# Kernel tuning notes

Measured on AMD Instinct MI355X. Metric: run time of the kernel, lower is better.

The kernel has to match this reference:

```python
import jax, jax.numpy as jnp
import numpy as np

N_NODES = 40000
N_EDGES = 640000
IN_DIM = 256
HID = 128
EMB = 128


def _mean_agg(h, src, dst, n):
    # PyG SimpleConv(aggr='mean'): out[i] = mean_{(j->i) in E} h[j]; 0 if no in-edges
    s = jax.ops.segment_sum(h[src], dst, num_segments=n)              # [N, D]
    deg = jax.ops.segment_sum(jnp.ones((src.shape[0],), h.dtype), dst,
                              num_segments=n)                          # [N]
    return s / jnp.maximum(deg, 1.0)[:, None]


def setup_inputs() -> dict:
    key = jax.random.key(0)
    ks = jax.random.split(key, 10)
    scale_in = 1.0 / np.sqrt(IN_DIM)
    scale_mix = 1.0 / np.sqrt(2 * HID)
    scale_out = 1.0 / np.sqrt(HID)
    return {
        "x": jax.random.normal(ks[0], (N_NODES, IN_DIM), dtype=jnp.float32),
        "W_in": jax.random.uniform(ks[1], (IN_DIM, HID), jnp.float32, -scale_in, scale_in),
        "b_in": jnp.zeros((HID,), jnp.float32),
        "W_mix0": jax.random.uniform(ks[2], (2 * HID, HID), jnp.float32, -scale_mix, scale_mix),
        "b_mix0": jnp.zeros((HID,), jnp.float32),
        "W_mix1": jax.random.uniform(ks[3], (2 * HID, HID), jnp.float32, -scale_mix, scale_mix),
        "b_mix1": jnp.zeros((HID,), jnp.float32),
        "W_out": jax.random.uniform(ks[4], (HID, EMB), jnp.float32, -scale_out, scale_out),
        "b_out": jnp.zeros((EMB,), jnp.float32),
        "edge_index": jax.random.randint(ks[5], (2, N_EDGES), 0, N_NODES, dtype=jnp.int64 if jax.config.jax_enable_x64 else jnp.int32),
    }


def reference(x, W_in, b_in, W_mix0, b_mix0, W_mix1, b_mix1, W_out, b_out, edge_index):
    src, dst = edge_index[0], edge_index[1]
    n = x.shape[0]
    # eval mode: dropout is identity
    h = jax.nn.relu(x @ W_in + b_in)                                   # [N, HID]
    for i, (W_mix, b_mix) in enumerate([(W_mix0, b_mix0), (W_mix1, b_mix1)]):
        h1 = _mean_agg(h, src, dst, n)                                 # 1-hop mean
        h2 = _mean_agg(h1, src, dst, n)                                # 2-hop mean
        h = jnp.concatenate([h1, h2], axis=-1) @ W_mix + b_mix         # [N, HID]
        if i != 1:
            h = jax.nn.relu(h)
    return h @ W_out + b_out                                           # [N, EMB]
```

## Files before the change

kernel.cpp:

```cpp
#include <hip/hip_runtime.h>

#define N_NODES 40000
#define N_EDGES 640000
#define IN_DIM 256
#define HID 128

typedef short bf16x8 __attribute__((ext_vector_type(8)));
typedef float f32x4 __attribute__((ext_vector_type(4)));

__device__ __forceinline__ unsigned short f2bf(float f) {
    unsigned int u = __float_as_uint(f);
    unsigned int r = (u + 0x7FFFu + ((u >> 16) & 1u)) >> 16;
    return (unsigned short)r;
}
__device__ __forceinline__ float bf2f(unsigned short b) {
    return __uint_as_float(((unsigned int)b) << 16);
}


__global__ __launch_bounds__(256) void front_kernel(
    const int* __restrict__ dst, int* __restrict__ deg, int E,
    const float* __restrict__ W0, const float* __restrict__ W1,
    const float* __restrict__ W2, const float* __restrict__ W3,
    unsigned short* __restrict__ H0, unsigned short* __restrict__ L0,
    unsigned short* __restrict__ H1, unsigned short* __restrict__ L1,
    unsigned short* __restrict__ H2, unsigned short* __restrict__ L2,
    unsigned short* __restrict__ H3, unsigned short* __restrict__ L3) {
    int bid = blockIdx.x;
    if (bid < 2500) {
        int e = bid * 256 + threadIdx.x;
        if (e < E) atomicAdd(&deg[dst[e]], 1);
        return;
    }
    int i = (bid - 2500) * 256 + threadIdx.x;
    const float* W;
    unsigned short *H, *L;
    int local;
    if (i < 32768)       { W = W0; H = H0; L = L0; local = i; }
    else if (i < 65536)  { W = W1; H = H1; L = L1; local = i - 32768; }
    else if (i < 98304)  { W = W2; H = H2; L = L2; local = i - 65536; }
    else if (i < 114688) { W = W3; H = H3; L = L3; local = i - 98304; }
    else return;
    int k = local >> 7, c = local & 127;
    float w = W[local];
    unsigned short h = f2bf(w);
    unsigned short l = f2bf(w - bf2f(h));
    int d = (k >> 5) * 4096 + c * 32 + (k & 31);
    H[d] = h;
    L[d] = l;
}


__global__ __launch_bounds__(1024) void write_offsets(const int* __restrict__ deg,
                                                      int* __restrict__ row_off,
                                                      int* __restrict__ cursor, int N) {
    __shared__ int sh[1024];
    int tid = threadIdx.x;
    int bid = blockIdx.x;
    int limit = bid << 10;
    int psum = 0;
    for (int j = tid * 4; j < limit; j += 4096) {
        int4 v = *(const int4*)&deg[j];
        psum += v.x + v.y + v.z + v.w;
    }
    sh[tid] = psum;
    __syncthreads();
#pragma unroll
    for (int o = 512; o > 0; o >>= 1) {
        if (tid < o) sh[tid] += sh[tid + o];
        __syncthreads();
    }
    int base = sh[0];
    __syncthreads();
    int i = limit + tid;
    int v = (i < N) ? deg[i] : 0;
    sh[tid] = v;
    __syncthreads();
#pragma unroll
    for (int off = 1; off < 1024; off <<= 1) {
        int t = (tid >= off) ? sh[tid - off] : 0;
        __syncthreads();
        sh[tid] += t;
        __syncthreads();
    }
    int excl = sh[tid] - v + base;
    if (i < N) {
        row_off[i] = excl;
        cursor[i] = excl;
    }
    if (i == N - 1) row_off[N] = excl + v;
}


__global__ __launch_bounds__(256) void scatter_gemm1(
    const int* __restrict__ src, const int* __restrict__ dst,
    int* __restrict__ cursor, int* __restrict__ csr, int E,
    const float* __restrict__ x,
    const unsigned short* __restrict__ Bth, const unsigned short* __restrict__ Btl,
    const float* __restrict__ bias, unsigned short* __restrict__ Cbf) {
    int bid = blockIdx.x;
    if (bid >= 625) {
        int e = (bid - 625) * 256 + threadIdx.x;
        if (e < E) {
            int p = atomicAdd(&cursor[dst[e]], 1);
            csr[p] = src[e];
        }
        return;
    }
    __shared__ unsigned short Ah[64 * 32], Al[64 * 32];
    __shared__ unsigned short Bh[128 * 32], Bl[128 * 32];
    int tid = threadIdx.x;
    int lane = tid & 63, wid = tid >> 6;
    int wr = wid >> 1, wc = wid & 1;
    int row0 = bid * 64;

    f32x4 acc[2][4];
#pragma unroll
    for (int rt = 0; rt < 2; ++rt)
#pragma unroll
        for (int ct = 0; ct < 4; ++ct) acc[rt][ct] = 0.f;

    for (int s = 0; s < 8; ++s) {
        int kbase = s * 32;
#pragma unroll
        for (int i = 0; i < 2; ++i) {
            int cch = tid + i * 256;
            int r = cch >> 3, q = cch & 7;
            float4 v = *(const float4*)&x[(size_t)(row0 + r) * IN_DIM + kbase + q * 4];
            ushort4 hh, ll;
            hh.x = f2bf(v.x); ll.x = f2bf(v.x - bf2f(hh.x));
            hh.y = f2bf(v.y); ll.y = f2bf(v.y - bf2f(hh.y));
            hh.z = f2bf(v.z); ll.z = f2bf(v.z - bf2f(hh.z));
            hh.w = f2bf(v.w); ll.w = f2bf(v.w - bf2f(hh.w));
            *(ushort4*)&Ah[r * 32 + q * 4] = hh;
            *(ushort4*)&Al[r * 32 + q * 4] = ll;
        }
        {
            const float4* sh4 = (const float4*)(Bth + s * 4096);
            const float4* sl4 = (const float4*)(Btl + s * 4096);
            float4* dh4 = (float4*)Bh;
            float4* dl4 = (float4*)Bl;
            dh4[tid] = sh4[tid];
            dh4[tid + 256] = sh4[tid + 256];
            dl4[tid] = sl4[tid];
            dl4[tid + 256] = sl4[tid + 256];
        }
        __syncthreads();

        bf16x8 afh[2], afl[2], bfh[4], bfl[4];
#pragma unroll
        for (int rt = 0; rt < 2; ++rt) {
            int off = (wr * 32 + rt * 16 + (lane & 15)) * 32 + (lane >> 4) * 8;
            afh[rt] = *(const bf16x8*)&Ah[off];
            afl[rt] = *(const bf16x8*)&Al[off];
        }
#pragma unroll
        for (int ct = 0; ct < 4; ++ct) {
            int off = (wc * 64 + ct * 16 + (lane & 15)) * 32 + (lane >> 4) * 8;
            bfh[ct] = *(const bf16x8*)&Bh[off];
            bfl[ct] = *(const bf16x8*)&Bl[off];
        }
#pragma unroll
        for (int rt = 0; rt < 2; ++rt)
#pragma unroll
            for (int ct = 0; ct < 4; ++ct) {
                acc[rt][ct] = __builtin_amdgcn_mfma_f32_16x16x32_bf16(afh[rt], bfh[ct], acc[rt][ct], 0, 0, 0);
                acc[rt][ct] = __builtin_amdgcn_mfma_f32_16x16x32_bf16(afh[rt], bfl[ct], acc[rt][ct], 0, 0, 0);
                acc[rt][ct] = __builtin_amdgcn_mfma_f32_16x16x32_bf16(afl[rt], bfh[ct], acc[rt][ct], 0, 0, 0);
            }
        __syncthreads();
    }

#pragma unroll
    for (int ct = 0; ct < 4; ++ct) {
        int col = wc * 64 + ct * 16 + (lane & 15);
        float bv = bias[col];
#pragma unroll
        for (int rt = 0; rt < 2; ++rt) {
#pragma unroll
            for (int r = 0; r < 4; ++r) {
                int row = row0 + wr * 32 + rt * 16 + (lane >> 4) * 4 + r;
                float v = fmaxf(acc[rt][ct][r] + bv, 0.f);
                Cbf[(size_t)row * 128 + col] = f2bf(v);
            }
        }
    }
}


__global__ __launch_bounds__(256) void agg_mean_bf(const unsigned short* __restrict__ hbf,
                                                   const int* __restrict__ row_off,
                                                   const int* __restrict__ csr,
                                                   unsigned short* __restrict__ out_bf,
                                                   int N) {
    int node = blockIdx.x * 4 + (threadIdx.x >> 6);
    if (node >= N) return;
    int lane = threadIdx.x & 63;
    int half = lane >> 5;
    int sub = lane & 31;
    int beg = row_off[node], end = row_off[node + 1];
    float4 a0 = make_float4(0.f, 0.f, 0.f, 0.f);
    float4 a1 = make_float4(0.f, 0.f, 0.f, 0.f);
    int e = beg;
    for (; e + 7 < end; e += 8) {
        int s0 = csr[e + half];
        int s1 = csr[e + 2 + half];
        int s2 = csr[e + 4 + half];
        int s3 = csr[e + 6 + half];
        ushort4 u0 = *(const ushort4*)&hbf[(size_t)s0 * HID + sub * 4];
        ushort4 u1 = *(const ushort4*)&hbf[(size_t)s1 * HID + sub * 4];
        ushort4 u2 = *(const ushort4*)&hbf[(size_t)s2 * HID + sub * 4];
        ushort4 u3 = *(const ushort4*)&hbf[(size_t)s3 * HID + sub * 4];
        a0.x += bf2f(u0.x) + bf2f(u2.x);
        a0.y += bf2f(u0.y) + bf2f(u2.y);
        a0.z += bf2f(u0.z) + bf2f(u2.z);
        a0.w += bf2f(u0.w) + bf2f(u2.w);
        a1.x += bf2f(u1.x) + bf2f(u3.x);
        a1.y += bf2f(u1.y) + bf2f(u3.y);
        a1.z += bf2f(u1.z) + bf2f(u3.z);
        a1.w += bf2f(u1.w) + bf2f(u3.w);
    }
    for (; e + half < end; e += 2) {
        int s = csr[e + half];
        ushort4 u = *(const ushort4*)&hbf[(size_t)s * HID + sub * 4];
        a0.x += bf2f(u.x);
        a0.y += bf2f(u.y);
        a0.z += bf2f(u.z);
        a0.w += bf2f(u.w);
    }
    float4 acc;
    acc.x = a0.x + a1.x;
    acc.y = a0.y + a1.y;
    acc.z = a0.z + a1.z;
    acc.w = a0.w + a1.w;
    acc.x += __shfl_xor(acc.x, 32);
    acc.y += __shfl_xor(acc.y, 32);
    acc.z += __shfl_xor(acc.z, 32);
    acc.w += __shfl_xor(acc.w, 32);
    if (half == 0) {
        float inv = 1.0f / fmaxf((float)(end - beg), 1.0f);
        ushort4 ub;
        ub.x = f2bf(acc.x * inv);
        ub.y = f2bf(acc.y * inv);
        ub.z = f2bf(acc.z * inv);
        ub.w = f2bf(acc.w * inv);
        *(ushort4*)&out_bf[(size_t)node * HID + sub * 4] = ub;
    }
}


template <bool RELU>
__global__ __launch_bounds__(256) void gemm_a16(
    const unsigned short* __restrict__ A0, const unsigned short* __restrict__ A1,
    const unsigned short* __restrict__ Bth, const unsigned short* __restrict__ Btl,
    const float* __restrict__ bias, unsigned short* __restrict__ Cbf) {
    __shared__ unsigned short Ab[64 * 32];
    __shared__ unsigned short Bh[128 * 32], Bl[128 * 32];
    int tid = threadIdx.x;
    int lane = tid & 63, wid = tid >> 6;
    int wr = wid >> 1, wc = wid & 1;
    int row0 = blockIdx.x * 64;

    f32x4 acc[2][4];
#pragma unroll
    for (int rt = 0; rt < 2; ++rt)
#pragma unroll
        for (int ct = 0; ct < 4; ++ct) acc[rt][ct] = 0.f;

    for (int s = 0; s < 8; ++s) {
        const unsigned short* Asrc = (s < 4) ? A0 : A1;
        int kbase = (s & 3) * 32;
        {
            int r = tid >> 2, q = (tid & 3) * 8;
            *(float4*)&Ab[r * 32 + q] =
                *(const float4*)&Asrc[(size_t)(row0 + r) * HID + kbase + q];
        }
        {
            const float4* sh4 = (const float4*)(Bth + s * 4096);
            const float4* sl4 = (const float4*)(Btl + s * 4096);
            float4* dh4 = (float4*)Bh;
            float4* dl4 = (float4*)Bl;
            dh4[tid] = sh4[tid];
            dh4[tid + 256] = sh4[tid + 256];
            dl4[tid] = sl4[tid];
            dl4[tid + 256] = sl4[tid + 256];
        }
        __syncthreads();

        bf16x8 af[2], bfh[4], bfl[4];
#pragma unroll
        for (int rt = 0; rt < 2; ++rt) {
            int off = (wr * 32 + rt * 16 + (lane & 15)) * 32 + (lane >> 4) * 8;
            af[rt] = *(const bf16x8*)&Ab[off];
        }
#pragma unroll
        for (int ct = 0; ct < 4; ++ct) {
            int off = (wc * 64 + ct * 16 + (lane & 15)) * 32 + (lane >> 4) * 8;
            bfh[ct] = *(const bf16x8*)&Bh[off];
            bfl[ct] = *(const bf16x8*)&Bl[off];
        }
#pragma unroll
        for (int rt = 0; rt < 2; ++rt)
#pragma unroll
            for (int ct = 0; ct < 4; ++ct) {
                acc[rt][ct] = __builtin_amdgcn_mfma_f32_16x16x32_bf16(af[rt], bfh[ct], acc[rt][ct], 0, 0, 0);
                acc[rt][ct] = __builtin_amdgcn_mfma_f32_16x16x32_bf16(af[rt], bfl[ct], acc[rt][ct], 0, 0, 0);
            }
        __syncthreads();
    }

#pragma unroll
    for (int ct = 0; ct < 4; ++ct) {
        int col = wc * 64 + ct * 16 + (lane & 15);
        float bv = bias[col];
#pragma unroll
        for (int rt = 0; rt < 2; ++rt) {
#pragma unroll
            for (int r = 0; r < 4; ++r) {
                int row = row0 + wr * 32 + rt * 16 + (lane >> 4) * 4 + r;
                float v = acc[rt][ct][r] + bv;
                if (RELU) v = fmaxf(v, 0.f);
                Cbf[(size_t)row * 128 + col] = f2bf(v);
            }
        }
    }
}


__global__ __launch_bounds__(256) void gemm_mix_out(
    const unsigned short* __restrict__ A0, const unsigned short* __restrict__ A1,
    const unsigned short* __restrict__ BmH, const unsigned short* __restrict__ BmL,
    const float* __restrict__ bias_m,
    const unsigned short* __restrict__ BoH, const unsigned short* __restrict__ BoL,
    const float* __restrict__ bias_o, float* __restrict__ out) {
    __shared__ unsigned short Ab[64 * 32];
    __shared__ unsigned short Bh[128 * 32], Bl[128 * 32];
    __shared__ unsigned short AoH[4][64 * 32], AoL[4][64 * 32];
    int tid = threadIdx.x;
    int lane = tid & 63, wid = tid >> 6;
    int wr = wid >> 1, wc = wid & 1;
    int row0 = blockIdx.x * 64;

    f32x4 acc[2][4];
#pragma unroll
    for (int rt = 0; rt < 2; ++rt)
#pragma unroll
        for (int ct = 0; ct < 4; ++ct) acc[rt][ct] = 0.f;

    for (int s = 0; s < 8; ++s) {
        const unsigned short* Asrc = (s < 4) ? A0 : A1;
        int kbase = (s & 3) * 32;
        {
            int r = tid >> 2, q = (tid & 3) * 8;
            *(float4*)&Ab[r * 32 + q] =
                *(const float4*)&Asrc[(size_t)(row0 + r) * HID + kbase + q];
        }
        {
            const float4* sh4 = (const float4*)(BmH + s * 4096);
            const float4* sl4 = (const float4*)(BmL + s * 4096);
            float4* dh4 = (float4*)Bh;
            float4* dl4 = (float4*)Bl;
            dh4[tid] = sh4[tid];
            dh4[tid + 256] = sh4[tid + 256];
            dl4[tid] = sl4[tid];
            dl4[tid + 256] = sl4[tid + 256];
        }
        __syncthreads();

        bf16x8 af[2], bfh[4], bfl[4];
#pragma unroll
        for (int rt = 0; rt < 2; ++rt) {
            int off = (wr * 32 + rt * 16 + (lane & 15)) * 32 + (lane >> 4) * 8;
            af[rt] = *(const bf16x8*)&Ab[off];
        }
#pragma unroll
        for (int ct = 0; ct < 4; ++ct) {
            int off = (wc * 64 + ct * 16 + (lane & 15)) * 32 + (lane >> 4) * 8;
            bfh[ct] = *(const bf16x8*)&Bh[off];
            bfl[ct] = *(const bf16x8*)&Bl[off];
        }
#pragma unroll
        for (int rt = 0; rt < 2; ++rt)
#pragma unroll
            for (int ct = 0; ct < 4; ++ct) {
                acc[rt][ct] = __builtin_amdgcn_mfma_f32_16x16x32_bf16(af[rt], bfh[ct], acc[rt][ct], 0, 0, 0);
                acc[rt][ct] = __builtin_amdgcn_mfma_f32_16x16x32_bf16(af[rt], bfl[ct], acc[rt][ct], 0, 0, 0);
            }
        __syncthreads();
    }

#pragma unroll
    for (int ct = 0; ct < 4; ++ct) {
        int c = wc * 64 + ct * 16 + (lane & 15);
        int sp = c >> 5, cc = c & 31;
        float bv = bias_m[c];
#pragma unroll
        for (int rt = 0; rt < 2; ++rt) {
#pragma unroll
            for (int r = 0; r < 4; ++r) {
                int rl = wr * 32 + rt * 16 + (lane >> 4) * 4 + r;
                float v = acc[rt][ct][r] + bv;
                unsigned short h = f2bf(v);
                unsigned short l = f2bf(v - bf2f(h));
                AoH[sp][rl * 32 + cc] = h;
                AoL[sp][rl * 32 + cc] = l;
            }
        }
    }

#pragma unroll
    for (int rt = 0; rt < 2; ++rt)
#pragma unroll
        for (int ct = 0; ct < 4; ++ct) acc[rt][ct] = 0.f;

    for (int s = 0; s < 4; ++s) {
        {
            const float4* sh4 = (const float4*)(BoH + s * 4096);
            const float4* sl4 = (const float4*)(BoL + s * 4096);
            float4* dh4 = (float4*)Bh;
            float4* dl4 = (float4*)Bl;
            dh4[tid] = sh4[tid];
            dh4[tid + 256] = sh4[tid + 256];
            dl4[tid] = sl4[tid];
            dl4[tid + 256] = sl4[tid + 256];
        }
        __syncthreads();

        bf16x8 afh[2], afl[2], bfh[4], bfl[4];
#pragma unroll
        for (int rt = 0; rt < 2; ++rt) {
            int off = (wr * 32 + rt * 16 + (lane & 15)) * 32 + (lane >> 4) * 8;
            afh[rt] = *(const bf16x8*)&AoH[s][off];
            afl[rt] = *(const bf16x8*)&AoL[s][off];
        }
#pragma unroll
        for (int ct = 0; ct < 4; ++ct) {
            int off = (wc * 64 + ct * 16 + (lane & 15)) * 32 + (lane >> 4) * 8;
            bfh[ct] = *(const bf16x8*)&Bh[off];
            bfl[ct] = *(const bf16x8*)&Bl[off];
        }
#pragma unroll
        for (int rt = 0; rt < 2; ++rt)
#pragma unroll
            for (int ct = 0; ct < 4; ++ct) {
                acc[rt][ct] = __builtin_amdgcn_mfma_f32_16x16x32_bf16(afh[rt], bfh[ct], acc[rt][ct], 0, 0, 0);
                acc[rt][ct] = __builtin_amdgcn_mfma_f32_16x16x32_bf16(afh[rt], bfl[ct], acc[rt][ct], 0, 0, 0);
                acc[rt][ct] = __builtin_amdgcn_mfma_f32_16x16x32_bf16(afl[rt], bfh[ct], acc[rt][ct], 0, 0, 0);
            }
        __syncthreads();
    }

#pragma unroll
    for (int ct = 0; ct < 4; ++ct) {
        int col = wc * 64 + ct * 16 + (lane & 15);
        float bv = bias_o[col];
#pragma unroll
        for (int rt = 0; rt < 2; ++rt) {
#pragma unroll
            for (int r = 0; r < 4; ++r) {
                int row = row0 + wr * 32 + rt * 16 + (lane >> 4) * 4 + r;
                out[(size_t)row * 128 + col] = acc[rt][ct][r] + bv;
            }
        }
    }
}


extern "C" void kernel_launch(void* const* d_in, const int* in_sizes, int n_in,
                              void* d_out, int out_size, void* d_ws, size_t ws_size,
                              hipStream_t stream) {
    const float* x     = (const float*)d_in[0];
    const float* W_in  = (const float*)d_in[1];
    const float* b_in  = (const float*)d_in[2];
    const float* W_m0  = (const float*)d_in[3];
    const float* b_m0  = (const float*)d_in[4];
    const float* W_m1  = (const float*)d_in[5];
    const float* b_m1  = (const float*)d_in[6];
    const float* W_o   = (const float*)d_in[7];
    const float* b_o   = (const float*)d_in[8];
    const int*   eidx  = (const int*)d_in[9];
    const int* src = eidx;
    const int* dst = eidx + N_EDGES;

    char* ws = (char*)d_ws;
    size_t off = 0;
    auto alloc = [&](size_t bytes) -> char* {
        char* p = ws + off;
        off += (bytes + 255) & ~(size_t)255;
        return p;
    };
    int* deg     = (int*)alloc((size_t)N_NODES * 4);
    int* row_off = (int*)alloc((size_t)(N_NODES + 1) * 4);
    int* cursor  = (int*)alloc((size_t)N_NODES * 4);
    int* csr     = (int*)alloc((size_t)N_EDGES * 4);
    unsigned short* hbf1 = (unsigned short*)alloc((size_t)N_NODES * HID * 2);
    unsigned short* hbf2 = (unsigned short*)alloc((size_t)N_NODES * HID * 2);
    unsigned short* hbf3 = (unsigned short*)alloc((size_t)N_NODES * HID * 2);
    unsigned short* WinH = (unsigned short*)alloc(32768 * 2);
    unsigned short* WinL = (unsigned short*)alloc(32768 * 2);
    unsigned short* Wm0H = (unsigned short*)alloc(32768 * 2);
    unsigned short* Wm0L = (unsigned short*)alloc(32768 * 2);
    unsigned short* Wm1H = (unsigned short*)alloc(32768 * 2);
    unsigned short* Wm1L = (unsigned short*)alloc(32768 * 2);
    unsigned short* WoH  = (unsigned short*)alloc(16384 * 2);
    unsigned short* WoL  = (unsigned short*)alloc(16384 * 2);
    (void)ws_size;

    const int NB = (N_NODES + 1023) / 1024;

    hipMemsetAsync(deg, 0, (size_t)N_NODES * 4, stream);
    front_kernel<<<2500 + 448, 256, 0, stream>>>(dst, deg, N_EDGES,
                                                 W_in, W_m0, W_m1, W_o,
                                                 WinH, WinL, Wm0H, Wm0L,
                                                 Wm1H, Wm1L, WoH, WoL);
    write_offsets<<<NB, 1024, 0, stream>>>(deg, row_off, cursor, N_NODES);

    scatter_gemm1<<<625 + 2500, 256, 0, stream>>>(src, dst, cursor, csr, N_EDGES,
                                                  x, WinH, WinL, b_in, hbf1);

    agg_mean_bf<<<10000, 256, 0, stream>>>(hbf1, row_off, csr, hbf2, N_NODES);
    agg_mean_bf<<<10000, 256, 0, stream>>>(hbf2, row_off, csr, hbf3, N_NODES);
    gemm_a16<true><<<625, 256, 0, stream>>>(hbf2, hbf3, Wm0H, Wm0L, b_m0, hbf1);

    agg_mean_bf<<<10000, 256, 0, stream>>>(hbf1, row_off, csr, hbf2, N_NODES);
    agg_mean_bf<<<10000, 256, 0, stream>>>(hbf2, row_off, csr, hbf3, N_NODES);

    gemm_mix_out<<<625, 256, 0, stream>>>(hbf2, hbf3, Wm1H, Wm1L, b_m1,
                                          WoH, WoL, b_o, (float*)d_out);
}
```

Measured before the change: 217.3 us.

## Build CSR via two-level bucketed counting sort instead of per-node global atomics

Replaces the per-edge global atomic degree count, the full-node scan and the per-edge global atomic scatter with a two-level bucket sort. Edges are first counted into 313 buckets of 128 destination nodes using shared-memory atomics, then scattered into a packed staging array. A per-bucket finalize kernel sorts each bucket locally to build row offsets and the CSR. This cuts contended global atomics and random global writes, at the cost of an extra kernel, a staging buffer, and packing src into 16 bits, which relies on N_NODES fitting in 16 bits.

```diff
diff --git a/kernel.cpp b/kernel.cpp
--- a/kernel.cpp
+++ b/kernel.cpp
@@ -4,6 +4,7 @@
 #define N_EDGES 640000
 #define IN_DIM 256
 #define HID 128
+#define NBUCK 313
 
 typedef short bf16x8 __attribute__((ext_vector_type(8)));
 typedef float f32x4 __attribute__((ext_vector_type(4)));
@@ -18,21 +19,28 @@
 }
 
 
-__global__ __launch_bounds__(256) void front_kernel(
-    const int* __restrict__ dst, int* __restrict__ deg, int E,
+__global__ __launch_bounds__(256) void count_prep(
+    const int* __restrict__ dst, int* __restrict__ gbcnt, int E,
     const float* __restrict__ W0, const float* __restrict__ W1,
     const float* __restrict__ W2, const float* __restrict__ W3,
     unsigned short* __restrict__ H0, unsigned short* __restrict__ L0,
     unsigned short* __restrict__ H1, unsigned short* __restrict__ L1,
     unsigned short* __restrict__ H2, unsigned short* __restrict__ L2,
     unsigned short* __restrict__ H3, unsigned short* __restrict__ L3) {
-    int bid = blockIdx.x;
-    if (bid < 2500) {
-        int e = bid * 256 + threadIdx.x;
-        if (e < E) atomicAdd(&deg[dst[e]], 1);
+    int bid = blockIdx.x, tid = threadIdx.x;
+    if (bid < 157) {
+        __shared__ int cnt[NBUCK];
+        for (int j = tid; j < NBUCK; j += 256) cnt[j] = 0;
+        __syncthreads();
+        int base = bid * 4096;
+        int lim = min(base + 4096, E);
+        for (int i = base + tid; i < lim; i += 256) atomicAdd(&cnt[dst[i] >> 7], 1);
+        __syncthreads();
+        for (int j = tid; j < NBUCK; j += 256)
+            if (cnt[j]) atomicAdd(&gbcnt[j], cnt[j]);
         return;
     }
-    int i = (bid - 2500) * 256 + threadIdx.x;
+    int i = (bid - 157) * 256 + tid;
     const float* W;
     unsigned short *H, *L;
     int local;
@@ -51,65 +59,63 @@
 }
 
 
-__global__ __launch_bounds__(1024) void write_offsets(const int* __restrict__ deg,
-                                                      int* __restrict__ row_off,
-                                                      int* __restrict__ cursor, int N) {
-    __shared__ int sh[1024];
+__global__ __launch_bounds__(512) void scan_buckets(const int* __restrict__ gbcnt,
+                                                    int* __restrict__ bbase,
+                                                    int* __restrict__ bcursor,
+                                                    int* __restrict__ row_off) {
+    __shared__ int sh[512];
     int tid = threadIdx.x;
-    int bid = blockIdx.x;
-    int limit = bid << 10;
-    int psum = 0;
-    for (int j = tid * 4; j < limit; j += 4096) {
-        int4 v = *(const int4*)&deg[j];
-        psum += v.x + v.y + v.z + v.w;
-    }
-    sh[tid] = psum;
-    __syncthreads();
-#pragma unroll
-    for (int o = 512; o > 0; o >>= 1) {
-        if (tid < o) sh[tid] += sh[tid + o];
-        __syncthreads();
-    }
-    int base = sh[0];
-    __syncthreads();
-    int i = limit + tid;
-    int v = (i < N) ? deg[i] : 0;
+    int v = (tid < NBUCK) ? gbcnt[tid] : 0;
     sh[tid] = v;
     __syncthreads();
 #pragma unroll
-    for (int off = 1; off < 1024; off <<= 1) {
+    for (int off = 1; off < 512; off <<= 1) {
         int t = (tid >= off) ? sh[tid - off] : 0;
         __syncthreads();
         sh[tid] += t;
         __syncthreads();
     }
-    int excl = sh[tid] - v + base;
-    if (i < N) {
-        row_off[i] = excl;
-        cursor[i] = excl;
-    }
-    if (i == N - 1) row_off[N] = excl + v;
+    int excl = sh[tid] - v;
+    if (tid < NBUCK) {
+        bbase[tid] = excl;
+        bcursor[tid] = excl;
+    }
+    if (tid == NBUCK - 1) bbase[NBUCK] = excl + v;
+    if (tid == 0) row_off[N_NODES] = N_EDGES;
 }
 
 
 __global__ __launch_bounds__(256) void scatter_gemm1(
     const int* __restrict__ src, const int* __restrict__ dst,
-    int* __restrict__ cursor, int* __restrict__ csr, int E,
+    int* __restrict__ bcursor, unsigned int* __restrict__ stage, int E,
     const float* __restrict__ x,
     const unsigned short* __restrict__ Bth, const unsigned short* __restrict__ Btl,
     const float* __restrict__ bias, unsigned short* __restrict__ Cbf) {
     int bid = blockIdx.x;
+    int tid = threadIdx.x;
     if (bid >= 625) {
-        int e = (bid - 625) * 256 + threadIdx.x;
-        if (e < E) {
-            int p = atomicAdd(&cursor[dst[e]], 1);
-            csr[p] = src[e];
+        __shared__ int cnt[NBUCK];
+        int b2 = bid - 625;
+        for (int j = tid; j < NBUCK; j += 256) cnt[j] = 0;
+        __syncthreads();
+        int base = b2 * 4096;
+        int lim = min(base + 4096, E);
+        for (int i = base + tid; i < lim; i += 256) atomicAdd(&cnt[dst[i] >> 7], 1);
+        __syncthreads();
+        for (int j = tid; j < NBUCK; j += 256) {
+            int c = cnt[j];
+            if (c) cnt[j] = atomicAdd(&bcursor[j], c);
+        }
+        __syncthreads();
+        for (int i = base + tid; i < lim; i += 256) {
+            unsigned int d = (unsigned int)dst[i];
+            int p = atomicAdd(&cnt[d >> 7], 1);
+            stage[p] = (d << 16) | (unsigned int)src[i];
         }
         return;
     }
     __shared__ unsigned short Ah[64 * 32], Al[64 * 32];
     __shared__ unsigned short Bh[128 * 32], Bl[128 * 32];
-    int tid = threadIdx.x;
     int lane = tid & 63, wid = tid >> 6;
     int wr = wid >> 1, wc = wid & 1;
     int row0 = bid * 64;
@@ -184,6 +190,45 @@
                 Cbf[(size_t)row * 128 + col] = f2bf(v);
             }
         }
+    }
+}
+
+
+__global__ __launch_bounds__(256) void finalize_csr(const unsigned int* __restrict__ stage,
+                                                    const int* __restrict__ bbase,
+                                                    int* __restrict__ row_off,
+                                                    int* __restrict__ csr) {
+    __shared__ int ncnt[128];
+    __shared__ int s2[128];
+    int b = blockIdx.x, tid = threadIdx.x;
+    int nbase = b << 7;
+    int ncount = min(128, N_NODES - nbase);
+    int ebase = bbase[b], eend = bbase[b + 1];
+    if (tid < 128) ncnt[tid] = 0;
+    __syncthreads();
+    for (int i = ebase + tid; i < eend; i += 256)
+        atomicAdd(&ncnt[(stage[i] >> 16) & 127], 1);
+    __syncthreads();
+    if (tid < 128) s2[tid] = ncnt[tid];
+    __syncthreads();
+#pragma unroll
+    for (int off = 1; off < 128; off <<= 1) {
+        int t = (tid < 128 && tid >= off) ? s2[tid - off] : 0;
+        __syncthreads();
+        if (tid < 128) s2[tid] += t;
+        __syncthreads();
+    }
+    if (tid < 128) {
+        int excl = s2[tid] - ncnt[tid];
+        if (tid < ncount) row_off[nbase + tid] = ebase + excl;
+        ncnt[tid] = excl;
+    }
+    __syncthreads();
+    for (int i = ebase + tid; i < eend; i += 256) {
+        unsigned int ent = stage[i];
+        int loc = (ent >> 16) & 127;
+        int p = atomicAdd(&ncnt[loc], 1);
+        csr[ebase + p] = (int)(ent & 0xFFFFu);
     }
 }
 
@@ -489,10 +534,12 @@
         off += (bytes + 255) & ~(size_t)255;
         return p;
     };
-    int* deg     = (int*)alloc((size_t)N_NODES * 4);
+    int* gbcnt   = (int*)alloc((size_t)NBUCK * 4);
+    int* bbase   = (int*)alloc((size_t)(NBUCK + 1) * 4);
+    int* bcursor = (int*)alloc((size_t)NBUCK * 4);
     int* row_off = (int*)alloc((size_t)(N_NODES + 1) * 4);
-    int* cursor  = (int*)alloc((size_t)N_NODES * 4);
     int* csr     = (int*)alloc((size_t)N_EDGES * 4);
+    unsigned int* stage = (unsigned int*)alloc((size_t)N_EDGES * 4);
     unsigned short* hbf1 = (unsigned short*)alloc((size_t)N_NODES * HID * 2);
     unsigned short* hbf2 = (unsigned short*)alloc((size_t)N_NODES * HID * 2);
     unsigned short* hbf3 = (unsigned short*)alloc((size_t)N_NODES * HID * 2);
@@ -506,17 +553,15 @@
     unsigned short* WoL  = (unsigned short*)alloc(16384 * 2);
     (void)ws_size;
 
-    const int NB = (N_NODES + 1023) / 1024;
-
-    hipMemsetAsync(deg, 0, (size_t)N_NODES * 4, stream);
-    front_kernel<<<2500 + 448, 256, 0, stream>>>(dst, deg, N_EDGES,
-                                                 W_in, W_m0, W_m1, W_o,
-                                                 WinH, WinL, Wm0H, Wm0L,
-                                                 Wm1H, Wm1L, WoH, WoL);
-    write_offsets<<<NB, 1024, 0, stream>>>(deg, row_off, cursor, N_NODES);
-
-    scatter_gemm1<<<625 + 2500, 256, 0, stream>>>(src, dst, cursor, csr, N_EDGES,
-                                                  x, WinH, WinL, b_in, hbf1);
+    hipMemsetAsync(gbcnt, 0, (size_t)NBUCK * 4, stream);
+    count_prep<<<157 + 448, 256, 0, stream>>>(dst, gbcnt, N_EDGES,
+                                              W_in, W_m0, W_m1, W_o,
+                                              WinH, WinL, Wm0H, Wm0L,
+                                              Wm1H, Wm1L, WoH, WoL);
+    scan_buckets<<<1, 512, 0, stream>>>(gbcnt, bbase, bcursor, row_off);
+    scatter_gemm1<<<625 + 157, 256, 0, stream>>>(src, dst, bcursor, stage, N_EDGES,
+                                                 x, WinH, WinL, b_in, hbf1);
+    finalize_csr<<<NBUCK, 256, 0, stream>>>(stage, bbase, row_off, csr);
 
     agg_mean_bf<<<10000, 256, 0, stream>>>(hbf1, row_off, csr, hbf2, N_NODES);
     agg_mean_bf<<<10000, 256, 0, stream>>>(hbf2, row_off, csr, hbf3, N_NODES);
```

Result: faster. 187.9 us (-13.5%).
